# Kernel optimization log

Measured on AMD Instinct MI355X. Metric: run time of the kernel, lower is better.

## Reference

```python
import jax, jax.numpy as jnp
import numpy as np

N_HEADS = 16
N_KV_HEADS = 4
HEAD_DIM = 128
ROPE_THETA = 10000.0


def _rope_cos_sin(seq_len, head_dim, dtype):
    inv_freq = 1.0 / (ROPE_THETA ** (jnp.arange(0, head_dim, 2, dtype=jnp.float32) / head_dim))
    angles = jnp.arange(seq_len, dtype=jnp.float32)[:, None] * inv_freq[None, :]  # [S, hd/2]
    return jnp.cos(angles).astype(dtype), jnp.sin(angles).astype(dtype)


def _apply_rope(t, cos, sin):
    # t: [B, S, H, hd]; interleaved-pair (complex) rotation, Llama style
    B, S, H, hd = t.shape
    tr = t.reshape(B, S, H, hd // 2, 2)
    t0, t1 = tr[..., 0], tr[..., 1]
    c = cos[None, :, None, :]
    s = sin[None, :, None, :]
    out = jnp.stack([t0 * c - t1 * s, t0 * s + t1 * c], axis=-1)
    return out.reshape(B, S, H, hd)


def setup_inputs() -> dict:
    key = jax.random.key(0)
    ks = jax.random.split(key, 5)
    B, S, D = 2, 2048, 2048
    scale = 0.02
    return {
        "x": jax.random.normal(ks[0], (B, S, D), dtype=jnp.float32),
        "wq": jax.random.normal(ks[1], (N_HEADS * HEAD_DIM, D), dtype=jnp.float32) * scale,
        "wk": jax.random.normal(ks[2], (N_KV_HEADS * HEAD_DIM, D), dtype=jnp.float32) * scale,
        "wv": jax.random.normal(ks[3], (N_KV_HEADS * HEAD_DIM, D), dtype=jnp.float32) * scale,
        "wo": jax.random.normal(ks[4], (D, N_HEADS * HEAD_DIM), dtype=jnp.float32) * scale,
    }


def reference(x, wq, wk, wv, wo):
    B, S, D = x.shape
    hd = HEAD_DIM
    # QKV projections (torch Linear: y = x @ W.T)
    q = (x @ wq.T).reshape(B, S, N_HEADS, hd)
    k = (x @ wk.T).reshape(B, S, N_KV_HEADS, hd)
    v = (x @ wv.T).reshape(B, S, N_KV_HEADS, hd)
    # RoPE on q, k
    cos, sin = _rope_cos_sin(S, hd, x.dtype)
    q = _apply_rope(q, cos, sin)
    k = _apply_rope(k, cos, sin)
    # GQA: repeat kv heads to match query heads
    rep = N_HEADS // N_KV_HEADS
    k = jnp.repeat(k, rep, axis=2)  # [B, S, H, hd]
    v = jnp.repeat(v, rep, axis=2)
    # Causal SDPA
    scores = jnp.einsum("bqhd,bkhd->bhqk", q, k) / jnp.sqrt(jnp.asarray(hd, x.dtype))
    causal = jnp.tril(jnp.ones((S, S), dtype=bool))
    scores = jnp.where(causal[None, None], scores, jnp.asarray(-1e30, x.dtype))
    attn = jax.nn.softmax(scores, axis=-1)
    out = jnp.einsum("bhqk,bkhd->bqhd", attn, v).reshape(B, S, N_HEADS * hd)
    return out @ wo.T
```

## Files before the change

### kernel.cpp

```cpp
#include <hip/hip_runtime.h>
#include <stdint.h>

typedef unsigned short u16;
typedef __attribute__((ext_vector_type(8))) __bf16 bf16x8;
typedef __attribute__((ext_vector_type(4))) float f32x4;

__device__ __forceinline__ u16 f2bf(float f) {
  union { float f; uint32_t u; } v; v.f = f;
  uint32_t u = v.u;
  uint32_t r = (u + 0x7fffu + ((u >> 16) & 1u)) >> 16;
  return (u16)r;
}
__device__ __forceinline__ float bf2f(u16 h) {
  union { uint32_t u; float f; } v; v.u = ((uint32_t)h) << 16;
  return v.f;
}

__device__ __forceinline__ void gld16(const void* g, void* l) {
  __builtin_amdgcn_global_load_lds(
      (__attribute__((address_space(1))) void*)(uintptr_t)g,
      (__attribute__((address_space(3))) void*)l,
      16, 0, 0);
}

__global__ __launch_bounds__(256) void cast_all(const float* __restrict__ x,
                                                const float* __restrict__ wq,
                                                const float* __restrict__ wk,
                                                const float* __restrict__ wv,
                                                const float* __restrict__ wo,
                                                u16* __restrict__ xb,
                                                u16* __restrict__ wqkv,
                                                u16* __restrict__ wob) {
  for (int i = blockIdx.x * 256 + threadIdx.x; i < 4718592; i += 2048 * 256) {
    const float* src; u16* dst; int loc, base;
    if (i < 2097152)      { src = x;  dst = xb;   loc = i;           base = 0; }
    else if (i < 3145728) { src = wq; dst = wqkv; loc = i - 2097152; base = 0; }
    else if (i < 3407872) { src = wk; dst = wqkv; loc = i - 3145728; base = 1048576; }
    else if (i < 3670016) { src = wv; dst = wqkv; loc = i - 3407872; base = 1310720; }
    else                  { src = wo; dst = wob;  loc = i - 3670016; base = 0; }
    float4 f = ((const float4*)src)[loc];
    ushort4 o;
    o.x = f2bf(f.x); o.y = f2bf(f.y); o.z = f2bf(f.z); o.w = f2bf(f.w);
    ((ushort4*)dst)[base + loc] = o;
  }
}

__global__ __launch_bounds__(256) void gemm_bt(const u16* __restrict__ A,
                                               const u16* __restrict__ B,
                                               void* __restrict__ C,
                                               u16* __restrict__ Vtg,
                                               int M, int N, int K, int out_f32,
                                               int do_rope)
{
  __shared__ u16 As[128 * 64];
  __shared__ u16 Bs[128 * 64];
  const int tid  = threadIdx.x;
  const int wave = tid >> 6, lane = tid & 63;
  const int col  = lane & 15, quad = lane >> 4;

  const int nwg = gridDim.x * gridDim.y;
  int flat = blockIdx.y * gridDim.x + blockIdx.x;
  int swz  = (nwg & 7) ? flat : ((flat & 7) * (nwg >> 3) + (flat >> 3));
  const int bm = swz / gridDim.x, bn = swz % gridDim.x;

  const int wm = (wave >> 1) * 64, wn = (wave & 1) * 64;
  const size_t arow0 = (size_t)bm * 128, brow0 = (size_t)bn * 128;

  const int sr = lane >> 3, pc = lane & 7;

  const f32x4 fz = {0.f, 0.f, 0.f, 0.f};
  f32x4 acc[4][4];
  for (int i = 0; i < 4; ++i)
    for (int j = 0; j < 4; ++j) acc[i][j] = fz;

  for (int k0 = 0; k0 < K; k0 += 64) {
    __syncthreads();
    #pragma unroll
    for (int i = 0; i < 4; ++i) {
      int rA = wave * 32 + i * 8 + sr;
      int lc = pc ^ (rA & 7);
      gld16(A + (arow0 + rA) * K + k0 + lc * 8, As + (wave * 32 + i * 8) * 64);
      gld16(B + (brow0 + rA) * K + k0 + lc * 8, Bs + (wave * 32 + i * 8) * 64);
    }
    __syncthreads();
    #pragma unroll
    for (int kk = 0; kk < 2; ++kk) {
      const int swzk = (((kk * 4 + quad) ^ (col & 7)) * 8);
      bf16x8 af[4];
      #pragma unroll
      for (int mt = 0; mt < 4; ++mt)
        af[mt] = *(const bf16x8*)&As[(wm + mt * 16 + col) * 64 + swzk];
      #pragma unroll
      for (int nt = 0; nt < 4; ++nt) {
        bf16x8 bf = *(const bf16x8*)&Bs[(wn + nt * 16 + col) * 64 + swzk];
        #pragma unroll
        for (int mt = 0; mt < 4; ++mt)
          acc[mt][nt] = __builtin_amdgcn_mfma_f32_16x16x32_bf16(af[mt], bf, acc[mt][nt], 0, 0, 0);
      }
    }
  }

  const float qscale = 0.12751744515623627f;
  #pragma unroll
  for (int mt = 0; mt < 4; ++mt)
    #pragma unroll
    for (int nt = 0; nt < 4; ++nt) {
      const size_t gcol = brow0 + wn + nt * 16 + col;
      const bool v_here    = do_rope && (gcol >= 2560);
      const bool rope_here = do_rope && (gcol < 2560);
      const int  d    = (int)(gcol & 127);
      const float osc = (gcol < 2048) ? qscale : 1.0f;
      const float inv = exp2f(-(float)(d >> 1) * 0.20762050593046f);
      const bool odd  = (d & 1) != 0;
      if (v_here) {
        const int vc  = (int)gcol - 2560;
        const int kvh = vc >> 7;
        const size_t grow0 = arow0 + wm + mt * 16 + quad * 4;
        const int bb = (int)(grow0 >> 11);
        const int s0 = (int)(grow0 & 2047);
        ushort4 o4;
        o4.x = f2bf(acc[mt][nt][0]);
        o4.y = f2bf(acc[mt][nt][1]);
        o4.z = f2bf(acc[mt][nt][2]);
        o4.w = f2bf(acc[mt][nt][3]);
        *(ushort4*)&Vtg[((size_t)((bb * 4 + kvh) * 128 + d)) * 2048 + s0] = o4;
        continue;
      }
      #pragma unroll
      for (int i = 0; i < 4; ++i) {
        size_t grow = arow0 + wm + mt * 16 + quad * 4 + i;
        float v = acc[mt][nt][i];
        if (rope_here) {
          float p = __shfl_xor(v, 1);
          float ang = (float)(int)(grow & 2047) * inv;
          float sn, cs;
          __sincosf(ang, &sn, &cs);
          v = odd ? (p * sn + v * cs) * osc : (v * cs - p * sn) * osc;
        }
        if (out_f32) ((float*)C)[grow * N + gcol] = v;
        else         ((u16*)C)[grow * N + gcol]   = f2bf(v);
      }
    }
}

__global__ __launch_bounds__(256) void gemm_bt_dbuf(const u16* __restrict__ A,
                                                    const u16* __restrict__ B,
                                                    float* __restrict__ C,
                                                    int M, int N, int K)
{
  __shared__ u16 As[2][128 * 64];
  __shared__ u16 Bs[2][128 * 64];
  const int tid  = threadIdx.x;
  const int wave = tid >> 6, lane = tid & 63;
  const int col  = lane & 15, quad = lane >> 4;

  const int nwg = gridDim.x * gridDim.y;
  int flat = blockIdx.y * gridDim.x + blockIdx.x;
  int swz  = (nwg & 7) ? flat : ((flat & 7) * (nwg >> 3) + (flat >> 3));
  const int bm = swz / gridDim.x, bn = swz % gridDim.x;

  const int wm = (wave >> 1) * 64, wn = (wave & 1) * 64;
  const size_t arow0 = (size_t)bm * 128, brow0 = (size_t)bn * 128;
  const int sr = lane >> 3, pc = lane & 7;

  const f32x4 fz = {0.f, 0.f, 0.f, 0.f};
  f32x4 acc[4][4];
  for (int i = 0; i < 4; ++i)
    for (int j = 0; j < 4; ++j) acc[i][j] = fz;

  #pragma unroll
  for (int i = 0; i < 4; ++i) {
    int rA = wave * 32 + i * 8 + sr;
    int lc = pc ^ (rA & 7);
    gld16(A + (arow0 + rA) * K + lc * 8, As[0] + (wave * 32 + i * 8) * 64);
    gld16(B + (brow0 + rA) * K + lc * 8, Bs[0] + (wave * 32 + i * 8) * 64);
  }

  const int T = K / 64;
  for (int t = 0; t < T; ++t) {
    __syncthreads();
    if (t + 1 < T) {
      const int k0 = (t + 1) * 64;
      u16* ad = As[(t + 1) & 1];
      u16* bd = Bs[(t + 1) & 1];
      #pragma unroll
      for (int i = 0; i < 4; ++i) {
        int rA = wave * 32 + i * 8 + sr;
        int lc = pc ^ (rA & 7);
        gld16(A + (arow0 + rA) * K + k0 + lc * 8, ad + (wave * 32 + i * 8) * 64);
        gld16(B + (brow0 + rA) * K + k0 + lc * 8, bd + (wave * 32 + i * 8) * 64);
      }
    }
    const u16* Ac = As[t & 1];
    const u16* Bc = Bs[t & 1];
    #pragma unroll
    for (int kk = 0; kk < 2; ++kk) {
      const int swzk = (((kk * 4 + quad) ^ (col & 7)) * 8);
      bf16x8 af[4];
      #pragma unroll
      for (int mt = 0; mt < 4; ++mt)
        af[mt] = *(const bf16x8*)&Ac[(wm + mt * 16 + col) * 64 + swzk];
      #pragma unroll
      for (int nt = 0; nt < 4; ++nt) {
        bf16x8 bf = *(const bf16x8*)&Bc[(wn + nt * 16 + col) * 64 + swzk];
        #pragma unroll
        for (int mt = 0; mt < 4; ++mt)
          acc[mt][nt] = __builtin_amdgcn_mfma_f32_16x16x32_bf16(af[mt], bf, acc[mt][nt], 0, 0, 0);
      }
    }
  }

  #pragma unroll
  for (int mt = 0; mt < 4; ++mt)
    #pragma unroll
    for (int nt = 0; nt < 4; ++nt)
      #pragma unroll
      for (int i = 0; i < 4; ++i) {
        size_t grow = arow0 + wm + mt * 16 + quad * 4 + i;
        size_t gcol = brow0 + wn + nt * 16 + col;
        C[grow * N + gcol] = acc[mt][nt][i];
      }
}

__global__ __launch_bounds__(256, 2) void attn_kernel(const u16* __restrict__ QKV,
                                                      const u16* __restrict__ Vtg,
                                                      u16* __restrict__ Ctx,
                                                      int B, int S)
{
  const int x = blockIdx.x;
  const int t = x >> 5, bh = x & 31;
  const int qt = (x < 256) ? (15 - t) : (t - 8);
  const int h = bh & 15, b = bh >> 4;
  const int tid  = threadIdx.x;
  const int wave = tid >> 6, lane = tid & 63;
  const int col  = lane & 15, quad = lane >> 4;
  const int q0   = qt * 128;
  const int kvh  = h >> 2;
  const int row0w = q0 + wave * 32;

  __shared__ u16 Ks[64 * 128];
  __shared__ u16 Vt[128 * 64];
  __shared__ u16 Ps[4][32 * 72];

  bf16x8 aq[2][4];
  #pragma unroll
  for (int mt = 0; mt < 2; ++mt)
    #pragma unroll
    for (int ks = 0; ks < 4; ++ks)
      aq[mt][ks] = *(const bf16x8*)(QKV + (size_t)(b * S + row0w + mt * 16 + col) * 3072
                                        + h * 128 + ks * 32 + quad * 8);

  const u16* KVb = QKV + (size_t)b * S * 3072 + 2048 + kvh * 128;
  const u16* Vtb = Vtg + ((size_t)(b * 4 + kvh) * 128) * S;
  u16* Pw = Ps[wave];

  const f32x4 fz = {0.f, 0.f, 0.f, 0.f};
  f32x4 o[2][8];
  #pragma unroll
  for (int mt = 0; mt < 2; ++mt)
    #pragma unroll
    for (int nc = 0; nc < 8; ++nc) o[mt][nc] = fz;
  float rs[2] = {0.f, 0.f};

  const int kt_max = 2 * qt + 1;

  for (int kt = 0; kt <= kt_max; ++kt) {
    __syncthreads();
    #pragma unroll
    for (int i = 0; i < 4; ++i) {
      int r = wave * 16 + i * 4 + (lane >> 4);
      int lc = (lane & 15) ^ (r & 15);
      gld16(KVb + (size_t)(kt * 64 + r) * 3072 + lc * 8, Ks + (wave * 16 + i * 4) * 128);
    }
    #pragma unroll
    for (int i = 0; i < 4; ++i) {
      int r = wave * 32 + i * 8 + (lane >> 3);
      int lc = (lane & 7) ^ (r & 7);
      gld16(Vtb + (size_t)r * S + kt * 64 + lc * 8, Vt + (wave * 32 + i * 8) * 64);
    }
    __syncthreads();

    if (kt * 64 > row0w + 31) continue;
    const bool need_mask = (kt * 64 + 63 > row0w);

    #pragma unroll
    for (int nt = 0; nt < 4; ++nt) {
      bf16x8 kA[4];
      #pragma unroll
      for (int ks = 0; ks < 4; ++ks)
        kA[ks] = *(const bf16x8*)&Ks[(nt * 16 + col) * 128 + (((ks * 4 + quad) ^ col) * 8)];
      #pragma unroll
      for (int mt = 0; mt < 2; ++mt) {
        f32x4 st = fz;
        #pragma unroll
        for (int ks = 0; ks < 4; ++ks)
          st = __builtin_amdgcn_mfma_f32_16x16x32_bf16(kA[ks], aq[mt][ks], st, 0, 0, 0);
        float pv[4];
        const int kbase = kt * 64 + nt * 16 + quad * 4;
        const int qrow  = row0w + mt * 16 + col;
        #pragma unroll
        for (int i = 0; i < 4; ++i) {
          float s = st[i];
          if (need_mask && (kbase + i > qrow)) s = -__builtin_inff();
          pv[i] = exp2f(s);
        }
        rs[mt] += (pv[0] + pv[1]) + (pv[2] + pv[3]);
        uint32_t d0 = (__float_as_uint(pv[0]) >> 16) | (__float_as_uint(pv[1]) & 0xffff0000u);
        uint32_t d1 = (__float_as_uint(pv[2]) >> 16) | (__float_as_uint(pv[3]) & 0xffff0000u);
        uint2 dd; dd.x = d0; dd.y = d1;
        *(uint2*)&Pw[(mt * 16 + col) * 72 + nt * 16 + quad * 4] = dd;
      }
    }
    __asm__ volatile("" ::: "memory");

    bf16x8 ap[2][2];
    #pragma unroll
    for (int mt = 0; mt < 2; ++mt)
      #pragma unroll
      for (int ks = 0; ks < 2; ++ks)
        ap[mt][ks] = *(const bf16x8*)&Pw[(mt * 16 + col) * 72 + ks * 32 + quad * 8];
    #pragma unroll
    for (int nc = 0; nc < 8; ++nc) {
      #pragma unroll
      for (int ks = 0; ks < 2; ++ks) {
        bf16x8 bv = *(const bf16x8*)&Vt[(nc * 16 + col) * 64 + (((ks * 4 + quad) ^ (col & 7)) * 8)];
        #pragma unroll
        for (int mt = 0; mt < 2; ++mt)
          o[mt][nc] = __builtin_amdgcn_mfma_f32_16x16x32_bf16(ap[mt][ks], bv, o[mt][nc], 0, 0, 0);
      }
    }
  }

  #pragma unroll
  for (int mt = 0; mt < 2; ++mt) {
    float v = rs[mt];
    v += __shfl_xor(v, 16);
    v += __shfl_xor(v, 32);
    float lv[4];
    #pragma unroll
    for (int i = 0; i < 4; ++i)
      lv[i] = 1.0f / __shfl(v, quad * 4 + i);
    #pragma unroll
    for (int nc = 0; nc < 8; ++nc)
      #pragma unroll
      for (int i = 0; i < 4; ++i) {
        int qg = row0w + mt * 16 + quad * 4 + i;
        Ctx[(size_t)(b * S + qg) * 2048 + h * 128 + nc * 16 + col] =
            f2bf(o[mt][nc][i] * lv[i]);
      }
  }
}

extern "C" void kernel_launch(void* const* d_in, const int* in_sizes, int n_in,
                              void* d_out, int out_size, void* d_ws, size_t ws_size,
                              hipStream_t stream) {
  const int B = 2, S = 2048, D = 2048;
  const int M = B * S;
  const int NQKV = 3072;

  const float* x  = (const float*)d_in[0];
  const float* wq = (const float*)d_in[1];
  const float* wk = (const float*)d_in[2];
  const float* wv = (const float*)d_in[3];
  const float* wo = (const float*)d_in[4];

  char* ws = (char*)d_ws;
  u16* xb    = (u16*)ws; ws += (size_t)M * D * 2;
  u16* wqkvb = (u16*)ws; ws += (size_t)NQKV * D * 2;
  u16* wob   = (u16*)ws; ws += (size_t)D * D * 2;
  u16* qkvb  = (u16*)ws; ws += (size_t)M * NQKV * 2;
  u16* vtg   = (u16*)ws; ws += (size_t)B * 4 * 128 * S * 2;
  u16* ctx   = (u16*)ws; ws += (size_t)M * D * 2;

  cast_all<<<2048, 256, 0, stream>>>(x, wq, wk, wv, wo, xb, wqkvb, wob);

  gemm_bt<<<dim3(NQKV / 128, M / 128), 256, 0, stream>>>(xb, wqkvb, qkvb, vtg, M, NQKV, D, 0, 1);

  attn_kernel<<<512, 256, 0, stream>>>(qkvb, vtg, ctx, B, S);

  gemm_bt_dbuf<<<dim3(D / 128, M / 128), 256, 0, stream>>>(ctx, wob, (float*)d_out, M, D, D);
}
```

Baseline: 287.3 us.

## Tile V per key block, load it to registers, double-buffer K in LDS

The projection epilogue now writes V transposed in per-64-key tiles, so each key tile of V is one contiguous block. The attention kernel drops the shared-memory V staging and has each wave load its V fragments straight from global memory into registers. K is double-buffered in LDS, with the next tile prefetched while the current one is consumed, so each iteration needs one barrier instead of two. The intent is to overlap K loads with compute and cut LDS traffic and barriers. In exchange, all four waves now fetch the same V tile from global/L2 redundantly, and register pressure rises from holding 16 V fragments.

```diff
diff --git a/kernel.cpp b/kernel.cpp
--- a/kernel.cpp
+++ b/kernel.cpp
@@ -113,8 +113,7 @@
       const float inv = exp2f(-(float)(d >> 1) * 0.20762050593046f);
       const bool odd  = (d & 1) != 0;
       if (v_here) {
-        const int vc  = (int)gcol - 2560;
-        const int kvh = vc >> 7;
+        const int kvh = (int)((gcol - 2560) >> 7);
         const size_t grow0 = arow0 + wm + mt * 16 + quad * 4;
         const int bb = (int)(grow0 >> 11);
         const int s0 = (int)(grow0 & 2047);
@@ -123,7 +122,7 @@
         o4.y = f2bf(acc[mt][nt][1]);
         o4.z = f2bf(acc[mt][nt][2]);
         o4.w = f2bf(acc[mt][nt][3]);
-        *(ushort4*)&Vtg[((size_t)((bb * 4 + kvh) * 128 + d)) * 2048 + s0] = o4;
+        *(ushort4*)&Vtg[(((size_t)(bb * 4 + kvh) * 32 + (s0 >> 6)) * 128 + d) * 64 + (s0 & 63)] = o4;
         continue;
       }
       #pragma unroll
@@ -238,8 +237,7 @@
   const int kvh  = h >> 2;
   const int row0w = q0 + wave * 32;
 
-  __shared__ u16 Ks[64 * 128];
-  __shared__ u16 Vt[128 * 64];
+  __shared__ u16 Ks[2][64 * 128];
   __shared__ u16 Ps[4][32 * 72];
 
   bf16x8 aq[2][4];
@@ -251,7 +249,7 @@
                                         + h * 128 + ks * 32 + quad * 8);
 
   const u16* KVb = QKV + (size_t)b * S * 3072 + 2048 + kvh * 128;
-  const u16* Vtb = Vtg + ((size_t)(b * 4 + kvh) * 128) * S;
+  const u16* Vtb = Vtg + (size_t)(b * 4 + kvh) * 32 * 128 * 64;
   u16* Pw = Ps[wave];
 
   const f32x4 fz = {0.f, 0.f, 0.f, 0.f};
@@ -264,31 +262,44 @@
 
   const int kt_max = 2 * qt + 1;
 
+  #pragma unroll
+  for (int i = 0; i < 4; ++i) {
+    int r = wave * 16 + i * 4 + (lane >> 4);
+    int lc = (lane & 15) ^ (r & 15);
+    gld16(KVb + (size_t)r * 3072 + lc * 8, Ks[0] + (wave * 16 + i * 4) * 128);
+  }
+
   for (int kt = 0; kt <= kt_max; ++kt) {
     __syncthreads();
-    #pragma unroll
-    for (int i = 0; i < 4; ++i) {
-      int r = wave * 16 + i * 4 + (lane >> 4);
-      int lc = (lane & 15) ^ (r & 15);
-      gld16(KVb + (size_t)(kt * 64 + r) * 3072 + lc * 8, Ks + (wave * 16 + i * 4) * 128);
-    }
-    #pragma unroll
-    for (int i = 0; i < 4; ++i) {
-      int r = wave * 32 + i * 8 + (lane >> 3);
-      int lc = (lane & 7) ^ (r & 7);
-      gld16(Vtb + (size_t)r * S + kt * 64 + lc * 8, Vt + (wave * 32 + i * 8) * 64);
-    }
-    __syncthreads();
+    if (kt < kt_max) {
+      u16* kdst = Ks[(kt + 1) & 1];
+      #pragma unroll
+      for (int i = 0; i < 4; ++i) {
+        int r = wave * 16 + i * 4 + (lane >> 4);
+        int lc = (lane & 15) ^ (r & 15);
+        gld16(KVb + (size_t)((kt + 1) * 64 + r) * 3072 + lc * 8,
+              kdst + (wave * 16 + i * 4) * 128);
+      }
+    }
 
     if (kt * 64 > row0w + 31) continue;
     const bool need_mask = (kt * 64 + 63 > row0w);
+    const u16* Kc = Ks[kt & 1];
+
+    bf16x8 bv[8][2];
+    #pragma unroll
+    for (int nc = 0; nc < 8; ++nc)
+      #pragma unroll
+      for (int ks = 0; ks < 2; ++ks)
+        bv[nc][ks] = *(const bf16x8*)(Vtb + ((size_t)kt * 128 + nc * 16 + col) * 64
+                                          + ks * 32 + quad * 8);
 
     #pragma unroll
     for (int nt = 0; nt < 4; ++nt) {
       bf16x8 kA[4];
       #pragma unroll
       for (int ks = 0; ks < 4; ++ks)
-        kA[ks] = *(const bf16x8*)&Ks[(nt * 16 + col) * 128 + (((ks * 4 + quad) ^ col) * 8)];
+        kA[ks] = *(const bf16x8*)&Kc[(nt * 16 + col) * 128 + (((ks * 4 + quad) ^ col) * 8)];
       #pragma unroll
       for (int mt = 0; mt < 2; ++mt) {
         f32x4 st = fz;
@@ -320,15 +331,12 @@
       for (int ks = 0; ks < 2; ++ks)
         ap[mt][ks] = *(const bf16x8*)&Pw[(mt * 16 + col) * 72 + ks * 32 + quad * 8];
     #pragma unroll
-    for (int nc = 0; nc < 8; ++nc) {
-      #pragma unroll
-      for (int ks = 0; ks < 2; ++ks) {
-        bf16x8 bv = *(const bf16x8*)&Vt[(nc * 16 + col) * 64 + (((ks * 4 + quad) ^ (col & 7)) * 8)];
+    for (int nc = 0; nc < 8; ++nc)
+      #pragma unroll
+      for (int ks = 0; ks < 2; ++ks)
         #pragma unroll
         for (int mt = 0; mt < 2; ++mt)
-          o[mt][nc] = __builtin_amdgcn_mfma_f32_16x16x32_bf16(ap[mt][ks], bv, o[mt][nc], 0, 0, 0);
-      }
-    }
+          o[mt][nc] = __builtin_amdgcn_mfma_f32_16x16x32_bf16(ap[mt][ks], bv[nc][ks], o[mt][nc], 0, 0, 0);
   }
 
   #pragma unroll
```

Measured after the change: 338.0 us. 17.7% more time.

## Split attention query tile across 8 waves of 16 rows each

Applied to the files above, without the earlier changes.

The attention kernel now runs 512 threads per block, and each of the 8 waves handles 16 query rows instead of 32. The K/V tile load is spread over twice as many waves, and the per-wave register footprint (Q fragments, output accumulators) is halved. This aims at more waves in flight and finer causal skipping per wave. In exchange each wave reloads the K/V fragments from LDS for half as many MFMAs, so LDS traffic per unit of compute doubles, and block-wide barriers now involve more waves.

```diff
diff --git a/kernel.cpp b/kernel.cpp
--- a/kernel.cpp
+++ b/kernel.cpp
@@ -222,7 +222,7 @@
       }
 }
 
-__global__ __launch_bounds__(256, 2) void attn_kernel(const u16* __restrict__ QKV,
+__global__ __launch_bounds__(512, 4) void attn_kernel(const u16* __restrict__ QKV,
                                                       const u16* __restrict__ Vtg,
                                                       u16* __restrict__ Ctx,
                                                       int B, int S)
@@ -236,51 +236,47 @@
   const int col  = lane & 15, quad = lane >> 4;
   const int q0   = qt * 128;
   const int kvh  = h >> 2;
-  const int row0w = q0 + wave * 32;
+  const int row0w = q0 + wave * 16;
 
   __shared__ u16 Ks[64 * 128];
   __shared__ u16 Vt[128 * 64];
-  __shared__ u16 Ps[4][32 * 72];
-
-  bf16x8 aq[2][4];
-  #pragma unroll
-  for (int mt = 0; mt < 2; ++mt)
-    #pragma unroll
-    for (int ks = 0; ks < 4; ++ks)
-      aq[mt][ks] = *(const bf16x8*)(QKV + (size_t)(b * S + row0w + mt * 16 + col) * 3072
-                                        + h * 128 + ks * 32 + quad * 8);
+  __shared__ u16 Ps[8][16 * 72];
+
+  bf16x8 aq[4];
+  #pragma unroll
+  for (int ks = 0; ks < 4; ++ks)
+    aq[ks] = *(const bf16x8*)(QKV + (size_t)(b * S + row0w + col) * 3072
+                                  + h * 128 + ks * 32 + quad * 8);
 
   const u16* KVb = QKV + (size_t)b * S * 3072 + 2048 + kvh * 128;
   const u16* Vtb = Vtg + ((size_t)(b * 4 + kvh) * 128) * S;
   u16* Pw = Ps[wave];
 
   const f32x4 fz = {0.f, 0.f, 0.f, 0.f};
-  f32x4 o[2][8];
-  #pragma unroll
-  for (int mt = 0; mt < 2; ++mt)
-    #pragma unroll
-    for (int nc = 0; nc < 8; ++nc) o[mt][nc] = fz;
-  float rs[2] = {0.f, 0.f};
+  f32x4 o[8];
+  #pragma unroll
+  for (int nc = 0; nc < 8; ++nc) o[nc] = fz;
+  float rs = 0.f;
 
   const int kt_max = 2 * qt + 1;
 
   for (int kt = 0; kt <= kt_max; ++kt) {
     __syncthreads();
     #pragma unroll
-    for (int i = 0; i < 4; ++i) {
-      int r = wave * 16 + i * 4 + (lane >> 4);
+    for (int i = 0; i < 2; ++i) {
+      int r = wave * 8 + i * 4 + (lane >> 4);
       int lc = (lane & 15) ^ (r & 15);
-      gld16(KVb + (size_t)(kt * 64 + r) * 3072 + lc * 8, Ks + (wave * 16 + i * 4) * 128);
-    }
-    #pragma unroll
-    for (int i = 0; i < 4; ++i) {
-      int r = wave * 32 + i * 8 + (lane >> 3);
+      gld16(KVb + (size_t)(kt * 64 + r) * 3072 + lc * 8, Ks + (wave * 8 + i * 4) * 128);
+    }
+    #pragma unroll
+    for (int i = 0; i < 2; ++i) {
+      int r = wave * 16 + i * 8 + (lane >> 3);
       int lc = (lane & 7) ^ (r & 7);
-      gld16(Vtb + (size_t)r * S + kt * 64 + lc * 8, Vt + (wave * 32 + i * 8) * 64);
-    }
-    __syncthreads();
-
-    if (kt * 64 > row0w + 31) continue;
+      gld16(Vtb + (size_t)r * S + kt * 64 + lc * 8, Vt + (wave * 16 + i * 8) * 64);
+    }
+    __syncthreads();
+
+    if (kt * 64 > row0w + 15) continue;
     const bool need_mask = (kt * 64 + 63 > row0w);
 
     #pragma unroll
@@ -289,51 +285,43 @@
       #pragma unroll
       for (int ks = 0; ks < 4; ++ks)
         kA[ks] = *(const bf16x8*)&Ks[(nt * 16 + col) * 128 + (((ks * 4 + quad) ^ col) * 8)];
-      #pragma unroll
-      for (int mt = 0; mt < 2; ++mt) {
-        f32x4 st = fz;
-        #pragma unroll
-        for (int ks = 0; ks < 4; ++ks)
-          st = __builtin_amdgcn_mfma_f32_16x16x32_bf16(kA[ks], aq[mt][ks], st, 0, 0, 0);
-        float pv[4];
-        const int kbase = kt * 64 + nt * 16 + quad * 4;
-        const int qrow  = row0w + mt * 16 + col;
-        #pragma unroll
-        for (int i = 0; i < 4; ++i) {
-          float s = st[i];
-          if (need_mask && (kbase + i > qrow)) s = -__builtin_inff();
-          pv[i] = exp2f(s);
-        }
-        rs[mt] += (pv[0] + pv[1]) + (pv[2] + pv[3]);
-        uint32_t d0 = (__float_as_uint(pv[0]) >> 16) | (__float_as_uint(pv[1]) & 0xffff0000u);
-        uint32_t d1 = (__float_as_uint(pv[2]) >> 16) | (__float_as_uint(pv[3]) & 0xffff0000u);
-        uint2 dd; dd.x = d0; dd.y = d1;
-        *(uint2*)&Pw[(mt * 16 + col) * 72 + nt * 16 + quad * 4] = dd;
-      }
+      f32x4 st = fz;
+      #pragma unroll
+      for (int ks = 0; ks < 4; ++ks)
+        st = __builtin_amdgcn_mfma_f32_16x16x32_bf16(kA[ks], aq[ks], st, 0, 0, 0);
+      float pv[4];
+      const int kbase = kt * 64 + nt * 16 + quad * 4;
+      const int qrow  = row0w + col;
+      #pragma unroll
+      for (int i = 0; i < 4; ++i) {
+        float s = st[i];
+        if (need_mask && (kbase + i > qrow)) s = -__builtin_inff();
+        pv[i] = exp2f(s);
+      }
+      rs += (pv[0] + pv[1]) + (pv[2] + pv[3]);
+      uint32_t d0 = (__float_as_uint(pv[0]) >> 16) | (__float_as_uint(pv[1]) & 0xffff0000u);
+      uint32_t d1 = (__float_as_uint(pv[2]) >> 16) | (__float_as_uint(pv[3]) & 0xffff0000u);
+      uint2 dd; dd.x = d0; dd.y = d1;
+      *(uint2*)&Pw[col * 72 + nt * 16 + quad * 4] = dd;
     }
     __asm__ volatile("" ::: "memory");
 
-    bf16x8 ap[2][2];
-    #pragma unroll
-    for (int mt = 0; mt < 2; ++mt)
-      #pragma unroll
-      for (int ks = 0; ks < 2; ++ks)
-        ap[mt][ks] = *(const bf16x8*)&Pw[(mt * 16 + col) * 72 + ks * 32 + quad * 8];
+    bf16x8 ap[2];
+    #pragma unroll
+    for (int ks = 0; ks < 2; ++ks)
+      ap[ks] = *(const bf16x8*)&Pw[col * 72 + ks * 32 + quad * 8];
     #pragma unroll
     for (int nc = 0; nc < 8; ++nc) {
       #pragma unroll
       for (int ks = 0; ks < 2; ++ks) {
         bf16x8 bv = *(const bf16x8*)&Vt[(nc * 16 + col) * 64 + (((ks * 4 + quad) ^ (col & 7)) * 8)];
-        #pragma unroll
-        for (int mt = 0; mt < 2; ++mt)
-          o[mt][nc] = __builtin_amdgcn_mfma_f32_16x16x32_bf16(ap[mt][ks], bv, o[mt][nc], 0, 0, 0);
-      }
-    }
-  }
-
-  #pragma unroll
-  for (int mt = 0; mt < 2; ++mt) {
-    float v = rs[mt];
+        o[nc] = __builtin_amdgcn_mfma_f32_16x16x32_bf16(ap[ks], bv, o[nc], 0, 0, 0);
+      }
+    }
+  }
+
+  {
+    float v = rs;
     v += __shfl_xor(v, 16);
     v += __shfl_xor(v, 32);
     float lv[4];
@@ -344,9 +332,9 @@
     for (int nc = 0; nc < 8; ++nc)
       #pragma unroll
       for (int i = 0; i < 4; ++i) {
-        int qg = row0w + mt * 16 + quad * 4 + i;
+        int qg = row0w + quad * 4 + i;
         Ctx[(size_t)(b * S + qg) * 2048 + h * 128 + nc * 16 + col] =
-            f2bf(o[mt][nc][i] * lv[i]);
+            f2bf(o[nc][i] * lv[i]);
       }
   }
 }
@@ -376,7 +364,7 @@
 
   gemm_bt<<<dim3(NQKV / 128, M / 128), 256, 0, stream>>>(xb, wqkvb, qkvb, vtg, M, NQKV, D, 0, 1);
 
-  attn_kernel<<<512, 256, 0, stream>>>(qkvb, vtg, ctx, B, S);
+  attn_kernel<<<512, 512, 0, stream>>>(qkvb, vtg, ctx, B, S);
 
   gemm_bt_dbuf<<<dim3(D / 128, M / 128), 256, 0, stream>>>(ctx, wob, (float*)d_out, M, D, D);
 }
```

After: 295.4 us. 1.03x slower.
